# Kernel tuning notes

Hardware: AMD Instinct MI355X
Metric: run time of the kernel (lower is better)

Reference implementation:

```python
import jax, jax.numpy as jnp
import numpy as np

B, N, H, A = 2048, 49, 1024, 512


def setup_inputs() -> dict:
    key = jax.random.key(0)
    ks = jax.random.split(key, 9)
    s_h = 1.0 / np.sqrt(H)
    s_a = 1.0 / np.sqrt(A)
    return {
        "hidden": jax.random.normal(ks[0], (B, H), jnp.float32),
        "img_features": jax.random.normal(ks[1], (B, N, H), jnp.float32),
        "coverage": jax.random.uniform(ks[2], (B, N), jnp.float32),
        "W_h": jax.random.uniform(ks[3], (H, A), jnp.float32, -s_h, s_h),
        "b_h": jax.random.uniform(ks[4], (A,), jnp.float32, -s_h, s_h),
        "W_img": jax.random.uniform(ks[5], (H, A), jnp.float32, -s_h, s_h),
        "b_img": jax.random.uniform(ks[6], (A,), jnp.float32, -s_h, s_h),
        "W_cov": jax.random.uniform(ks[7], (1, A), jnp.float32, -1.0, 1.0),
        "v": jax.random.uniform(ks[8], (A,), jnp.float32, -s_a, s_a),
    }


def reference(hidden, img_features, coverage, W_h, b_h, W_img, b_img, W_cov, v):
    # h_proj: (B, 1, A); img_proj: (B, N, A)
    h_proj = (hidden @ W_h + b_h)[:, None, :]
    img_proj = jnp.einsum("bnh,ha->bna", img_features, W_img) + b_img
    # coverage projection: (B, N, 1) @ (1, A) -> (B, N, A)
    cov_proj = coverage[:, :, None] * W_cov[0]
    energy = jnp.tanh(h_proj + img_proj + cov_proj)
    scores = jnp.einsum("bna,a->bn", energy, v)  # (B, N)
    alpha = jax.nn.softmax(scores, axis=1)
    context = jnp.einsum("bn,bnh->bh", alpha, img_features)
    return (context, alpha)
```

## Files before the change

### kernel.cpp

```cpp
#include <hip/hip_runtime.h>
#include <cstdint>
#include <cstddef>

#define B_ 2048
#define N_ 49
#define H_ 1024
#define A_ 512
#define M_ (B_*N_)

typedef __attribute__((ext_vector_type(8))) short short8;
typedef __attribute__((ext_vector_type(8))) unsigned short ushort8;
typedef __attribute__((ext_vector_type(4))) float f32x4;
typedef unsigned int u32;

__device__ inline unsigned short f2bf(float f){
  union { float f; unsigned u; } v; v.f = f;
  unsigned r = v.u + 0x7FFFu + ((v.u >> 16) & 1u);
  return (unsigned short)(r >> 16);
}
__device__ inline float bf2f(unsigned short h){
  union { u32 u; float f; } v; v.u = ((u32)h) << 16; return v.f;
}
__device__ inline float fast_tanh(float x){
  float e = __expf(2.0f*x);
  return 1.0f - 2.0f/(e + 1.0f);
}
__device__ inline void gl16(const void* g, void* l){
  __builtin_amdgcn_global_load_lds((const __attribute__((address_space(1))) u32*)g,
                                   (__attribute__((address_space(3))) u32*)l, 16, 0, 0);
}

__global__ __launch_bounds__(256) void k_transpose(
    const float* __restrict__ Wh, const float* __restrict__ Wimg,
    unsigned short* __restrict__ WtH, unsigned short* __restrict__ WtImg){
  const float* src = blockIdx.y ? Wimg : Wh;
  unsigned short* dst = blockIdx.y ? WtImg : WtH;
  int tk = (blockIdx.x & 31) * 32;
  int ta = (blockIdx.x >> 5) * 32;
  __shared__ unsigned short tile[32][33];
  int t = threadIdx.x;
  int r = t >> 3, c4 = t & 7;
  float4 vv = *(const float4*)(src + (size_t)(tk + r)*A_ + ta + c4*4);
  tile[c4*4+0][r] = f2bf(vv.x);
  tile[c4*4+1][r] = f2bf(vv.y);
  tile[c4*4+2][r] = f2bf(vv.z);
  tile[c4*4+3][r] = f2bf(vv.w);
  __syncthreads();
  ushort4 o;
  o.x = tile[r][c4*4+0]; o.y = tile[r][c4*4+1];
  o.z = tile[r][c4*4+2]; o.w = tile[r][c4*4+3];
  *(ushort4*)(dst + (size_t)(ta + r)*H_ + tk + c4*4) = o;
}

__global__ __launch_bounds__(256) void k_convert(
    const float* __restrict__ src, unsigned short* __restrict__ dst, size_t n8){
  size_t i = (size_t)blockIdx.x*256 + threadIdx.x;
  size_t stride = (size_t)gridDim.x*256;
  const float4* s4 = (const float4*)src;
  ushort8* d8 = (ushort8*)dst;
  for (; i < n8; i += stride){
    float4 a = s4[2*i], b = s4[2*i+1];
    ushort8 o;
    o[0]=f2bf(a.x); o[1]=f2bf(a.y); o[2]=f2bf(a.z); o[3]=f2bf(a.w);
    o[4]=f2bf(b.x); o[5]=f2bf(b.y); o[6]=f2bf(b.z); o[7]=f2bf(b.w);
    d8[i] = o;
  }
}

#define BK 64
#define LDK 72

__device__ inline void gemm_tile(const float* __restrict__ Asrc,
                                 const unsigned short* __restrict__ Wt,
                                 int m0, int a0, f32x4 acc[4][4],
                                 unsigned short (*sA)[LDK], unsigned short (*sB)[LDK]){
  const int t = threadIdx.x;
  const int l = t & 63, w = t >> 6;
  const int wr = w >> 1, wc = w & 1;
  const int g = l >> 4, c = l & 15;
  #pragma unroll
  for (int m=0;m<4;m++)
    #pragma unroll
    for (int n=0;n<4;n++)
      acc[m][n] = f32x4{0.f,0.f,0.f,0.f};

  for (int k0 = 0; k0 < H_; k0 += BK){
    #pragma unroll
    for (int i=0;i<8;i++){
      int f = i*256 + t;
      int row = f >> 4, c4 = f & 15;
      float4 vv = *(const float4*)(Asrc + (size_t)(m0+row)*H_ + k0 + c4*4);
      ushort4 h; h.x=f2bf(vv.x); h.y=f2bf(vv.y); h.z=f2bf(vv.z); h.w=f2bf(vv.w);
      *(ushort4*)&sA[row][c4*4] = h;
    }
    #pragma unroll
    for (int i=0;i<8;i++){
      int f = i*256 + t;
      int row = f >> 4, c4 = f & 15;
      *(ushort4*)&sB[row][c4*4] = *(const ushort4*)(Wt + (size_t)(a0+row)*H_ + k0 + c4*4);
    }
    __syncthreads();
    #pragma unroll
    for (int kk=0; kk<BK; kk+=32){
      short8 aF[4], bF[4];
      #pragma unroll
      for (int m=0;m<4;m++) aF[m] = *(const short8*)&sA[wr*64 + m*16 + c][kk + g*8];
      #pragma unroll
      for (int n=0;n<4;n++) bF[n] = *(const short8*)&sB[wc*64 + n*16 + c][kk + g*8];
      #pragma unroll
      for (int m=0;m<4;m++)
        #pragma unroll
        for (int n=0;n<4;n++)
          acc[m][n] = __builtin_amdgcn_mfma_f32_16x16x32_bf16(aF[m], bF[n], acc[m][n], 0, 0, 0);
    }
    __syncthreads();
  }
}

__global__ __launch_bounds__(256) void k_hproj(
    const float* __restrict__ hidden, const unsigned short* __restrict__ WtH,
    const float* __restrict__ b_h, float* __restrict__ hproj){
  __shared__ __align__(16) unsigned short sA[128][LDK];
  __shared__ __align__(16) unsigned short sB[128][LDK];
  f32x4 acc[4][4];
  int m0 = blockIdx.x * 128, a0 = blockIdx.y * 128;
  gemm_tile(hidden, WtH, m0, a0, acc, sA, sB);
  const int l = threadIdx.x & 63, w = threadIdx.x >> 6;
  const int wr = w >> 1, wc = w & 1, g = l >> 4, c = l & 15;
  #pragma unroll
  for (int n=0;n<4;n++){
    int col = a0 + wc*64 + n*16 + c;
    float bh = b_h[col];
    #pragma unroll
    for (int m=0;m<4;m++)
      #pragma unroll
      for (int r=0;r<4;r++){
        int rowg = m0 + wr*64 + m*16 + g*4 + r;
        hproj[(size_t)rowg*A_ + col] = acc[m][n][r] + bh;
      }
  }
}

__global__ __launch_bounds__(512, 2) void k_scores_b2p(
    const unsigned short* __restrict__ Ab, const unsigned short* __restrict__ Wt,
    const float* __restrict__ hproj, const float* __restrict__ b_img,
    const float* __restrict__ cov, const float* __restrict__ Wcov,
    const float* __restrict__ v, float* __restrict__ scoresP){
  __shared__ __align__(16) char lds[131072];
  const int t = threadIdx.x;
  const int l = t & 63, w = t >> 6;
  const int wr = w >> 2, wc = w & 3;
  const int g = l >> 4, c = l & 15;
  const int cm = (c & 7) << 4;

  const int nwg = (M_/256)*(A_/256);
  int bid = blockIdx.x;
  int wg = (bid & 7)*(nwg/8) + (bid >> 3);
  const int m0 = (wg >> 1) * 256;
  const int a0 = (wg & 1) * 256;

  const int rsub = l >> 3;
  const int ksw  = ((l & 7) ^ rsub) * 8;

  f32x4 acc[8][4] = {};

  auto stage = [&](int bn, int k0){
    #pragma unroll
    for (int h=0; h<2; h++){
      #pragma unroll
      for (int q=0; q<2; q++){
        int dA = bn*65536 + h*16384 + w*2048 + q*1024;
        const unsigned short* ga = Ab + (size_t)(m0 + h*128 + w*16 + q*8 + rsub)*H_ + k0 + ksw;
        const unsigned short* gb = Wt + (size_t)(a0 + h*128 + w*16 + q*8 + rsub)*H_ + k0 + ksw;
        gl16(ga, lds + dA);
        gl16(gb, lds + dA + 32768);
      }
    }
  };

  const int abase = wr*16384;
  const int bbase = 32768 + (wc>>1)*16384;
  const int brow  = (wc&1)*64;

  stage(0, 0);
  for (int tt=0; tt<16; tt++){
    const int cur = (tt & 1) << 16;
    if (tt < 15){
      stage((tt+1)&1, (tt+1)*64);
      asm volatile("s_waitcnt vmcnt(8)" ::: "memory");
    } else {
      asm volatile("s_waitcnt vmcnt(0)" ::: "memory");
    }
    asm volatile("s_barrier" ::: "memory");
    #pragma unroll
    for (int p=0; p<4; p++){
      const int mh  = p >> 1;
      const int kb  = (p & 1) * 64;
      short8 aF[4], bF[4];
      #pragma unroll
      for (int i=0;i<4;i++){
        int rl = (mh*4+i)*16 + c;
        aF[i] = *(const short8*)(lds + cur + abase + rl*128 + ((kb + g*16) ^ cm));
      }
      #pragma unroll
      for (int n=0;n<4;n++){
        int rb = brow + n*16 + c;
        bF[n] = *(const short8*)(lds + cur + bbase + rb*128 + ((kb + g*16) ^ cm));
      }
      __builtin_amdgcn_s_setprio(1);
      #pragma unroll
      for (int i=0;i<4;i++)
        #pragma unroll
        for (int n=0;n<4;n++)
          acc[mh*4+i][n] = __builtin_amdgcn_mfma_f32_16x16x32_bf16(aF[i], bF[n], acc[mh*4+i][n], 0, 0, 0);
      __builtin_amdgcn_s_setprio(0);
    }
    asm volatile("s_barrier" ::: "memory");
  }

  float* sS = (float*)lds;
  float* sH = (float*)lds + 256;
  const int bFirst = m0 / N_;
  const int nB = (m0 + 255)/N_ - bFirst + 1;
  if (t < 256) sS[t] = 0.f;
  for (int idx = t; idx < nB*256; idx += 512){
    int bb = idx >> 8, a = idx & 255;
    sH[bb*256 + a] = hproj[(size_t)(bFirst + bb)*A_ + a0 + a];
  }
  __syncthreads();

  float vv[4], bi[4], wcv[4];
  #pragma unroll
  for (int n=0;n<4;n++){
    int colg = a0 + wc*64 + n*16 + c;
    vv[n] = v[colg]; bi[n] = b_img[colg]; wcv[n] = Wcov[colg];
  }
  #pragma unroll
  for (int m=0;m<8;m++){
    #pragma unroll
    for (int r=0;r<4;r++){
      int rowl = wr*128 + m*16 + g*4 + r;
      int rowg = m0 + rowl;
      int bb = rowg / N_ - bFirst;
      float cv = cov[rowg];
      float s = 0.f;
      #pragma unroll
      for (int n=0;n<4;n++){
        float x = acc[m][n][r] + sH[bb*256 + wc*64 + n*16 + c] + bi[n] + cv*wcv[n];
        s += fast_tanh(x) * vv[n];
      }
      s += __shfl_xor(s, 1, 16);
      s += __shfl_xor(s, 2, 16);
      s += __shfl_xor(s, 4, 16);
      s += __shfl_xor(s, 8, 16);
      if (c == 0) atomicAdd(&sS[rowl], s);
    }
  }
  __syncthreads();
  if (t < 256) scoresP[(size_t)(a0 >> 8)*M_ + m0 + t] = sS[t];
}

__global__ __launch_bounds__(256) void k_scores_f(
    const float* __restrict__ img, const unsigned short* __restrict__ WtImg,
    const float* __restrict__ hproj, const float* __restrict__ b_img,
    const float* __restrict__ cov, const float* __restrict__ Wcov,
    const float* __restrict__ v, float* __restrict__ scores){
  __shared__ __align__(16) unsigned short sA[128][LDK];
  __shared__ __align__(16) unsigned short sB[128][LDK];
  __shared__ float sH[4][128];
  f32x4 acc[4][4];
  int m0 = blockIdx.x * 128, a0 = blockIdx.y * 128;
  gemm_tile(img, WtImg, m0, a0, acc, sA, sB);
  int bFirst = m0 / N_;
  int bLast  = (m0 + 127) / N_;
  int nB = bLast - bFirst + 1;
  for (int idx = threadIdx.x; idx < nB*128; idx += 256){
    int bb = idx >> 7, a = idx & 127;
    sH[bb][a] = hproj[(size_t)(bFirst + bb)*A_ + a0 + a];
  }
  __syncthreads();
  const int l = threadIdx.x & 63, w = threadIdx.x >> 6;
  const int wr = w >> 1, wc = w & 1, g = l >> 4, c = l & 15;
  float vv[4], bi[4], wcv[4];
  #pragma unroll
  for (int n=0;n<4;n++){
    int col = a0 + wc*64 + n*16 + c;
    vv[n] = v[col]; bi[n] = b_img[col]; wcv[n] = Wcov[col];
  }
  #pragma unroll
  for (int m=0;m<4;m++)
    #pragma unroll
    for (int r=0;r<4;r++){
      int rowg = m0 + wr*64 + m*16 + g*4 + r;
      int bb = rowg / N_;
      float cv = cov[rowg];
      float s = 0.f;
      #pragma unroll
      for (int n=0;n<4;n++){
        float x = acc[m][n][r] + sH[bb - bFirst][wc*64 + n*16 + c] + bi[n] + cv*wcv[n];
        s += fast_tanh(x) * vv[n];
      }
      s += __shfl_xor(s, 1, 16);
      s += __shfl_xor(s, 2, 16);
      s += __shfl_xor(s, 4, 16);
      s += __shfl_xor(s, 8, 16);
      if (c == 0) atomicAdd(&scores[rowg], s);
    }
}

__global__ __launch_bounds__(256) void k_ctx_b(
    const unsigned short* __restrict__ imgb, const float* __restrict__ scoresP,
    float* __restrict__ outCtx, float* __restrict__ outAlpha){
  int b = blockIdx.x;
  __shared__ float sAl[N_];
  int t = threadIdx.x;
  if (t < 64){
    float s = -1e30f;
    if (t < N_){
      size_t rg = (size_t)b*N_ + t;
      s = scoresP[rg] + scoresP[(size_t)M_ + rg];
    }
    float m = s;
    #pragma unroll
    for (int off=32; off>=1; off>>=1) m = fmaxf(m, __shfl_xor(m, off));
    float e = (t < N_) ? __expf(s - m) : 0.f;
    float sum = e;
    #pragma unroll
    for (int off=32; off>=1; off>>=1) sum += __shfl_xor(sum, off);
    float al = e / sum;
    if (t < N_){ sAl[t] = al; outAlpha[(size_t)b*N_ + t] = al; }
  }
  __syncthreads();
  float4 acc = {0.f,0.f,0.f,0.f};
  #pragma unroll 7
  for (int n=0;n<N_;n++){
    float al = sAl[n];
    ushort4 x = *(const ushort4*)(imgb + ((size_t)b*N_ + n)*H_ + t*4);
    acc.x += al*bf2f(x.x); acc.y += al*bf2f(x.y);
    acc.z += al*bf2f(x.z); acc.w += al*bf2f(x.w);
  }
  *(float4*)(outCtx + (size_t)b*H_ + t*4) = acc;
}

__global__ __launch_bounds__(256) void k_ctx_f(
    const float* __restrict__ img, const float* __restrict__ scores,
    float* __restrict__ outCtx, float* __restrict__ outAlpha){
  int b = blockIdx.x;
  __shared__ float sAl[N_];
  int t = threadIdx.x;
  if (t < 64){
    float s = (t < N_) ? scores[(size_t)b*N_ + t] : -1e30f;
    float m = s;
    #pragma unroll
    for (int off=32; off>=1; off>>=1) m = fmaxf(m, __shfl_xor(m, off));
    float e = (t < N_) ? __expf(s - m) : 0.f;
    float sum = e;
    #pragma unroll
    for (int off=32; off>=1; off>>=1) sum += __shfl_xor(sum, off);
    float al = e / sum;
    if (t < N_){ sAl[t] = al; outAlpha[(size_t)b*N_ + t] = al; }
  }
  __syncthreads();
  const float4* ib = (const float4*)(img + (size_t)b*N_*H_);
  float4 acc = {0.f,0.f,0.f,0.f};
  for (int n=0;n<N_;n++){
    float al = sAl[n];
    float4 x = ib[n*(H_/4) + t];
    acc.x += al*x.x; acc.y += al*x.y; acc.z += al*x.z; acc.w += al*x.w;
  }
  *(float4*)(outCtx + (size_t)b*H_ + t*4) = acc;
}

extern "C" void kernel_launch(void* const* d_in, const int* in_sizes, int n_in,
                              void* d_out, int out_size, void* d_ws, size_t ws_size,
                              hipStream_t stream){
  const float* hidden = (const float*)d_in[0];
  const float* img    = (const float*)d_in[1];
  const float* cov    = (const float*)d_in[2];
  const float* W_h    = (const float*)d_in[3];
  const float* b_h    = (const float*)d_in[4];
  const float* W_img  = (const float*)d_in[5];
  const float* b_img  = (const float*)d_in[6];
  const float* W_cov  = (const float*)d_in[7];
  const float* v      = (const float*)d_in[8];

  char* ws = (char*)d_ws;
  unsigned short* WtH   = (unsigned short*)ws;
  unsigned short* WtImg = (unsigned short*)(ws + (1u<<20));
  float* hproj   = (float*)(ws + (2u<<20));
  float* scoresP = (float*)(ws + (6u<<20));
  unsigned short* imgb = (unsigned short*)(ws + (8u<<20));

  float* outCtx   = (float*)d_out;
  float* outAlpha = outCtx + (size_t)B_*H_;

  const size_t needed = (8ull<<20) + (size_t)M_*H_*2;

  k_transpose<<<dim3(512, 2), 256, 0, stream>>>(W_h, W_img, WtH, WtImg);
  k_hproj<<<dim3(B_/128, A_/128), 256, 0, stream>>>(hidden, WtH, b_h, hproj);

  if (ws_size >= needed){
    k_convert<<<2048, 256, 0, stream>>>(img, imgb, (size_t)M_*H_/8);
    k_scores_b2p<<<(M_/256)*(A_/256), 512, 0, stream>>>(imgb, WtImg, hproj, b_img, cov, W_cov, v, scoresP);
    k_ctx_b<<<B_, 256, 0, stream>>>(imgb, scoresP, outCtx, outAlpha);
  } else {
    hipMemsetAsync(scoresP, 0, (size_t)M_*sizeof(float), stream);
    k_scores_f<<<dim3(M_/128, A_/128), 256, 0, stream>>>(img, WtImg, hproj, b_img, cov, W_cov, v, scoresP);
    k_ctx_f<<<B_, 256, 0, stream>>>(img, scoresP, outCtx, outAlpha);
  }
}
```

Measured before the change: 371.4 us.

## Fuse fp32-to-bf16 image conversion into the scores GEMM A-operand loading

Removes the separate conversion kernel. The scores GEMM now reads fp32 img rows into registers, converts them to bf16 with v_cvt_pk_bf16_f32, writes them to swizzled LDS, and the a0==0 workgroup also writes the bf16 copy out for the context kernel. This drops one full write-then-read pass of the bf16 image through memory, but the GEMM now reads fp32 (twice the bytes) from both column halves. Register-staged loads also replace direct global-to-LDS loads, which raises register pressure and weakens the pipelining.

Result: slower. 393.5 us (+5.9%).

```diff
diff --git a/kernel.cpp b/kernel.cpp
--- a/kernel.cpp
+++ b/kernel.cpp
@@ -52,21 +52,6 @@
   *(ushort4*)(dst + (size_t)(ta + r)*H_ + tk + c4*4) = o;
 }
 
-__global__ __launch_bounds__(256) void k_convert(
-    const float* __restrict__ src, unsigned short* __restrict__ dst, size_t n8){
-  size_t i = (size_t)blockIdx.x*256 + threadIdx.x;
-  size_t stride = (size_t)gridDim.x*256;
-  const float4* s4 = (const float4*)src;
-  ushort8* d8 = (ushort8*)dst;
-  for (; i < n8; i += stride){
-    float4 a = s4[2*i], b = s4[2*i+1];
-    ushort8 o;
-    o[0]=f2bf(a.x); o[1]=f2bf(a.y); o[2]=f2bf(a.z); o[3]=f2bf(a.w);
-    o[4]=f2bf(b.x); o[5]=f2bf(b.y); o[6]=f2bf(b.z); o[7]=f2bf(b.w);
-    d8[i] = o;
-  }
-}
-
 #define BK 64
 #define LDK 72
 
@@ -141,11 +126,12 @@
   }
 }
 
-__global__ __launch_bounds__(512, 2) void k_scores_b2p(
-    const unsigned short* __restrict__ Ab, const unsigned short* __restrict__ Wt,
-    const float* __restrict__ hproj, const float* __restrict__ b_img,
-    const float* __restrict__ cov, const float* __restrict__ Wcov,
-    const float* __restrict__ v, float* __restrict__ scoresP){
+__global__ __launch_bounds__(512, 2) void k_scores_r(
+    const float* __restrict__ img, unsigned short* __restrict__ imgb,
+    const unsigned short* __restrict__ Wt, const float* __restrict__ hproj,
+    const float* __restrict__ b_img, const float* __restrict__ cov,
+    const float* __restrict__ Wcov, const float* __restrict__ v,
+    float* __restrict__ scoresP){
   __shared__ __align__(16) char lds[131072];
   const int t = threadIdx.x;
   const int l = t & 63, w = t >> 6;
@@ -158,55 +144,61 @@
   int wg = (bid & 7)*(nwg/8) + (bid >> 3);
   const int m0 = (wg >> 1) * 256;
   const int a0 = (wg & 1) * 256;
+  const bool wrImg = (a0 == 0);
 
   const int rsub = l >> 3;
   const int ksw  = ((l & 7) ^ rsub) * 8;
+  const int arow = t >> 1, akq = t & 1;
+  const int awsw = (arow & 7) << 4;
 
   f32x4 acc[8][4] = {};
-
-  auto stage = [&](int bn, int k0){
-    #pragma unroll
-    for (int h=0; h<2; h++){
-      #pragma unroll
-      for (int q=0; q<2; q++){
-        int dA = bn*65536 + h*16384 + w*2048 + q*1024;
-        const unsigned short* ga = Ab + (size_t)(m0 + h*128 + w*16 + q*8 + rsub)*H_ + k0 + ksw;
-        const unsigned short* gb = Wt + (size_t)(a0 + h*128 + w*16 + q*8 + rsub)*H_ + k0 + ksw;
-        gl16(ga, lds + dA);
-        gl16(gb, lds + dA + 32768);
+  float4 av[8];
+
+  auto loadA = [&](int k0){
+    const float4* p = (const float4*)(img + (size_t)(m0 + arow)*H_ + k0 + akq*32);
+    #pragma unroll
+    for (int i=0;i<8;i++) av[i] = p[i];
+  };
+  auto stageB = [&](int bn, int k0){
+    #pragma unroll
+    for (int h=0;h<2;h++)
+      #pragma unroll
+      for (int q=0;q<2;q++){
+        int row = h*128 + w*16 + q*8 + rsub;
+        gl16(Wt + (size_t)(a0 + row)*H_ + k0 + ksw,
+             lds + bn*65536 + 32768 + h*16384 + w*2048 + q*1024);
       }
-    }
   };
-
-  const int abase = wr*16384;
-  const int bbase = 32768 + (wc>>1)*16384;
-  const int brow  = (wc&1)*64;
-
-  stage(0, 0);
-  for (int tt=0; tt<16; tt++){
+  auto writeA = [&](int bn, int k0){
+    unsigned short* gb = imgb + (size_t)(m0 + arow)*H_ + k0 + akq*32;
+    #pragma unroll
+    for (int j=0;j<4;j++){
+      union { short8 s; u32 u[4]; } pk;
+      float4 lo = av[2*j], hi = av[2*j+1];
+      asm("v_cvt_pk_bf16_f32 %0, %1, %2" : "=v"(pk.u[0]) : "v"(lo.x), "v"(lo.y));
+      asm("v_cvt_pk_bf16_f32 %0, %1, %2" : "=v"(pk.u[1]) : "v"(lo.z), "v"(lo.w));
+      asm("v_cvt_pk_bf16_f32 %0, %1, %2" : "=v"(pk.u[2]) : "v"(hi.x), "v"(hi.y));
+      asm("v_cvt_pk_bf16_f32 %0, %1, %2" : "=v"(pk.u[3]) : "v"(hi.z), "v"(hi.w));
+      *(short8*)(lds + bn*65536 + arow*128 + ((akq*64 + j*16) ^ awsw)) = pk.s;
+      if (wrImg) *(short8*)(gb + j*8) = pk.s;
+    }
+  };
+  auto compute = [&](int tt){
     const int cur = (tt & 1) << 16;
-    if (tt < 15){
-      stage((tt+1)&1, (tt+1)*64);
-      asm volatile("s_waitcnt vmcnt(8)" ::: "memory");
-    } else {
-      asm volatile("s_waitcnt vmcnt(0)" ::: "memory");
-    }
-    asm volatile("s_barrier" ::: "memory");
+    const int abase = cur + wr*16384;
+    const int bbase = cur + 32768 + (wc>>1)*16384;
+    const int brow  = (wc & 1)*64;
     #pragma unroll
     for (int p=0; p<4; p++){
-      const int mh  = p >> 1;
-      const int kb  = (p & 1) * 64;
+      const int mh = p >> 1;
+      const int kb = (p & 1) * 64;
       short8 aF[4], bF[4];
       #pragma unroll
-      for (int i=0;i<4;i++){
-        int rl = (mh*4+i)*16 + c;
-        aF[i] = *(const short8*)(lds + cur + abase + rl*128 + ((kb + g*16) ^ cm));
-      }
-      #pragma unroll
-      for (int n=0;n<4;n++){
-        int rb = brow + n*16 + c;
-        bF[n] = *(const short8*)(lds + cur + bbase + rb*128 + ((kb + g*16) ^ cm));
-      }
+      for (int i=0;i<4;i++)
+        aF[i] = *(const short8*)(lds + abase + ((mh*4+i)*16 + c)*128 + ((kb + g*16) ^ cm));
+      #pragma unroll
+      for (int n=0;n<4;n++)
+        bF[n] = *(const short8*)(lds + bbase + (brow + n*16 + c)*128 + ((kb + g*16) ^ cm));
       __builtin_amdgcn_s_setprio(1);
       #pragma unroll
       for (int i=0;i<4;i++)
@@ -214,6 +206,33 @@
         for (int n=0;n<4;n++)
           acc[mh*4+i][n] = __builtin_amdgcn_mfma_f32_16x16x32_bf16(aF[i], bF[n], acc[mh*4+i][n], 0, 0, 0);
       __builtin_amdgcn_s_setprio(0);
+    }
+  };
+
+  loadA(0);
+  stageB(0, 0);
+  asm volatile("s_waitcnt vmcnt(4)" ::: "memory");
+  writeA(0, 0);
+  asm volatile("s_waitcnt lgkmcnt(0)" ::: "memory");
+  if (wrImg) asm volatile("s_waitcnt vmcnt(4)" ::: "memory");
+  else       asm volatile("s_waitcnt vmcnt(0)" ::: "memory");
+  asm volatile("s_barrier" ::: "memory");
+
+  for (int tt=0; tt<16; ++tt){
+    if (tt < 15){
+      loadA((tt+1)*64);
+      stageB((tt+1)&1, (tt+1)*64);
+      asm volatile("" ::: "memory");
+    }
+    compute(tt);
+    if (tt < 15){
+      asm volatile("s_waitcnt vmcnt(4)" ::: "memory");
+      writeA((tt+1)&1, (tt+1)*64);
+      asm volatile("s_waitcnt lgkmcnt(0)" ::: "memory");
+      if (wrImg) asm volatile("s_waitcnt vmcnt(4)" ::: "memory");
+      else       asm volatile("s_waitcnt vmcnt(0)" ::: "memory");
+    } else {
+      asm volatile("s_waitcnt vmcnt(0)" ::: "memory");
     }
     asm volatile("s_barrier" ::: "memory");
   }
@@ -240,9 +259,8 @@
     #pragma unroll
     for (int r=0;r<4;r++){
       int rowl = wr*128 + m*16 + g*4 + r;
-      int rowg = m0 + rowl;
-      int bb = rowg / N_ - bFirst;
-      float cv = cov[rowg];
+      int bb = (m0 + rowl) / N_ - bFirst;
+      float cv = cov[m0 + rowl];
       float s = 0.f;
       #pragma unroll
       for (int n=0;n<4;n++){
@@ -258,6 +276,40 @@
   }
   __syncthreads();
   if (t < 256) scoresP[(size_t)(a0 >> 8)*M_ + m0 + t] = sS[t];
+}
+
+__global__ __launch_bounds__(256) void k_ctx_b(
+    const unsigned short* __restrict__ imgb, const float* __restrict__ scoresP,
+    float* __restrict__ outCtx, float* __restrict__ outAlpha){
+  int b = blockIdx.x;
+  __shared__ float sAl[N_];
+  int t = threadIdx.x;
+  if (t < 64){
+    float s = -1e30f;
+    if (t < N_){
+      size_t rg = (size_t)b*N_ + t;
+      s = scoresP[rg] + scoresP[(size_t)M_ + rg];
+    }
+    float m = s;
+    #pragma unroll
+    for (int off=32; off>=1; off>>=1) m = fmaxf(m, __shfl_xor(m, off));
+    float e = (t < N_) ? __expf(s - m) : 0.f;
+    float sum = e;
+    #pragma unroll
+    for (int off=32; off>=1; off>>=1) sum += __shfl_xor(sum, off);
+    float al = e / sum;
+    if (t < N_){ sAl[t] = al; outAlpha[(size_t)b*N_ + t] = al; }
+  }
+  __syncthreads();
+  float4 acc = {0.f,0.f,0.f,0.f};
+  #pragma unroll 7
+  for (int n=0;n<N_;n++){
+    float al = sAl[n];
+    ushort4 x = *(const ushort4*)(imgb + ((size_t)b*N_ + n)*H_ + t*4);
+    acc.x += al*bf2f(x.x); acc.y += al*bf2f(x.y);
+    acc.z += al*bf2f(x.z); acc.w += al*bf2f(x.w);
+  }
+  *(float4*)(outCtx + (size_t)b*H_ + t*4) = acc;
 }
 
 __global__ __launch_bounds__(256) void k_scores_f(
@@ -308,40 +360,6 @@
     }
 }
 
-__global__ __launch_bounds__(256) void k_ctx_b(
-    const unsigned short* __restrict__ imgb, const float* __restrict__ scoresP,
-    float* __restrict__ outCtx, float* __restrict__ outAlpha){
-  int b = blockIdx.x;
-  __shared__ float sAl[N_];
-  int t = threadIdx.x;
-  if (t < 64){
-    float s = -1e30f;
-    if (t < N_){
-      size_t rg = (size_t)b*N_ + t;
-      s = scoresP[rg] + scoresP[(size_t)M_ + rg];
-    }
-    float m = s;
-    #pragma unroll
-    for (int off=32; off>=1; off>>=1) m = fmaxf(m, __shfl_xor(m, off));
-    float e = (t < N_) ? __expf(s - m) : 0.f;
-    float sum = e;
-    #pragma unroll
-    for (int off=32; off>=1; off>>=1) sum += __shfl_xor(sum, off);
-    float al = e / sum;
-    if (t < N_){ sAl[t] = al; outAlpha[(size_t)b*N_ + t] = al; }
-  }
-  __syncthreads();
-  float4 acc = {0.f,0.f,0.f,0.f};
-  #pragma unroll 7
-  for (int n=0;n<N_;n++){
-    float al = sAl[n];
-    ushort4 x = *(const ushort4*)(imgb + ((size_t)b*N_ + n)*H_ + t*4);
-    acc.x += al*bf2f(x.x); acc.y += al*bf2f(x.y);
-    acc.z += al*bf2f(x.z); acc.w += al*bf2f(x.w);
-  }
-  *(float4*)(outCtx + (size_t)b*H_ + t*4) = acc;
-}
-
 __global__ __launch_bounds__(256) void k_ctx_f(
     const float* __restrict__ img, const float* __restrict__ scores,
     float* __restrict__ outCtx, float* __restrict__ outAlpha){
@@ -400,8 +418,7 @@
   k_hproj<<<dim3(B_/128, A_/128), 256, 0, stream>>>(hidden, WtH, b_h, hproj);
 
   if (ws_size >= needed){
-    k_convert<<<2048, 256, 0, stream>>>(img, imgb, (size_t)M_*H_/8);
-    k_scores_b2p<<<(M_/256)*(A_/256), 512, 0, stream>>>(imgb, WtImg, hproj, b_img, cov, W_cov, v, scoresP);
+    k_scores_r<<<(M_/256)*(A_/256), 512, 0, stream>>>(img, imgb, WtImg, hproj, b_img, cov, W_cov, v, scoresP);
     k_ctx_b<<<B_, 256, 0, stream>>>(imgb, scoresP, outCtx, outAlpha);
   } else {
     hipMemsetAsync(scoresP, 0, (size_t)M_*sizeof(float), stream);
```
